# Optimization experiments

Measured on AMD Instinct MI355X. Metric: run time of the kernel, lower is better.

Reference implementation:

```python
import jax, jax.numpy as jnp
import numpy as np

D_MODEL = 1024
NUM_HEADS = 16
HEAD_DIM = D_MODEL // NUM_HEADS
B, S = 2, 2048


def setup_inputs() -> dict:
    key = jax.random.key(0)
    ks = jax.random.split(key, 16)
    sd = 1.0 / np.sqrt(D_MODEL)
    def lin(k):
        kw, kb = jax.random.split(k)
        W = jax.random.uniform(kw, (D_MODEL, D_MODEL), jnp.float32, -sd, sd)
        b = jax.random.uniform(kb, (D_MODEL,), jnp.float32, -sd, sd)
        return W, b
    Wq, bq = lin(ks[0]); Wk, bk = lin(ks[1]); Wv, bv = lin(ks[2]); Wo, bo = lin(ks[3])
    return {
        'q': jax.random.normal(ks[4], (B, S, D_MODEL), jnp.float32),
        'k': jax.random.normal(ks[5], (B, S, D_MODEL), jnp.float32),
        'v': jax.random.normal(ks[6], (B, S, D_MODEL), jnp.float32),
        'phase': jax.random.normal(ks[7], (B,), jnp.float32),
        'Wq': Wq, 'bq': bq, 'Wk': Wk, 'bk': bk, 'Wv': Wv, 'bv': bv, 'Wo': Wo, 'bo': bo,
        'phase_coupling': jnp.zeros((1, NUM_HEADS, 1, 1), jnp.float32),
        'attention_scale': jnp.ones((1,), jnp.float32),
        'stability_factor': jnp.ones((1,), jnp.float32),
    }


def reference(q, k, v, phase, Wq, bq, Wk, bk, Wv, bv, Wo, bo,
              phase_coupling, attention_scale, stability_factor):
    batch, seq, _ = q.shape
    scale = HEAD_DIM ** -0.5

    def split_heads(x):  # [B,S,D] -> [B,H,S,hd]
        return x.reshape(batch, -1, NUM_HEADS, HEAD_DIM).transpose(0, 2, 1, 3)

    qh = split_heads(q @ Wq.T + bq)
    kh = split_heads(k @ Wk.T + bk)
    vh = split_heads(v @ Wv.T + bv)

    scores = jnp.einsum('bhqd,bhkd->bhqk', qh, kh) * (scale * attention_scale)
    # phase modulation: phase [B] -> [B,1,1,1]; scores *= 1 + coupling*sin(phase)
    phase_factor = jnp.sin(phase)[:, None, None, None]
    scores = scores * (1.0 + phase_coupling * phase_factor)

    attn_weights = jax.nn.softmax(scores, axis=-1)  # dropout is identity in eval
    out = jnp.einsum('bhqk,bhkd->bhqd', attn_weights, vh)
    out = out.transpose(0, 2, 1, 3).reshape(batch, seq, D_MODEL)
    out = (out @ Wo.T + bo) * stability_factor
    return out, attn_weights
```

## Files before the change

kernel.cpp:

```cpp
#include <hip/hip_runtime.h>
#include <hip/hip_bf16.h>
#include <cstdint>
#include <cstddef>
#include <cmath>

#define NH 16
#define HD 64
#define SS 2048
#define DM 1024
#define MTOT 4096

typedef __attribute__((ext_vector_type(8))) short short8;
typedef __attribute__((ext_vector_type(4))) float float4v;
typedef __attribute__((ext_vector_type(4))) int int4v;
typedef __attribute__((ext_vector_type(4))) unsigned short ushort4v;

__device__ __forceinline__ unsigned short f2bf(float f){
  unsigned int u = __builtin_bit_cast(unsigned int, f);
  u += 0x7FFFu + ((u >> 16) & 1u);
  return (unsigned short)(u >> 16);
}

__device__ __forceinline__ void gload16(const void* g, void* l){
  __builtin_amdgcn_global_load_lds((const __attribute__((address_space(1))) void*)g,
                                   (__attribute__((address_space(3))) void*)l, 16, 0, 0);
}

__global__ __launch_bounds__(256) void cvt3_kernel(
    const float* __restrict__ s0, const float* __restrict__ s1, const float* __restrict__ s2,
    unsigned short* __restrict__ d0, unsigned short* __restrict__ d1, unsigned short* __restrict__ d2,
    int n){
  const int z = blockIdx.z;
  const float* src = z==0 ? s0 : (z==1 ? s1 : s2);
  unsigned short* dst = z==0 ? d0 : (z==1 ? d1 : d2);
  for (int i = (blockIdx.x*blockDim.x + threadIdx.x)*4; i < n; i += gridDim.x*blockDim.x*4){
    float4v v = *reinterpret_cast<const float4v*>(src + i);
    ushort4v o;
    o.x = f2bf(v.x); o.y = f2bf(v.y); o.z = f2bf(v.z); o.w = f2bf(v.w);
    *reinterpret_cast<ushort4v*>(dst + i) = o;
  }
}

__global__ __launch_bounds__(256) void cvt4_kernel(
    const float* __restrict__ s0, const float* __restrict__ s1,
    const float* __restrict__ s2, const float* __restrict__ s3,
    unsigned short* __restrict__ d0, unsigned short* __restrict__ d1,
    unsigned short* __restrict__ d2, unsigned short* __restrict__ d3,
    int n){
  const int z = blockIdx.z;
  const float* src = z==0 ? s0 : (z==1 ? s1 : (z==2 ? s2 : s3));
  unsigned short* dst = z==0 ? d0 : (z==1 ? d1 : (z==2 ? d2 : d3));
  for (int i = (blockIdx.x*blockDim.x + threadIdx.x)*4; i < n; i += gridDim.x*blockDim.x*4){
    float4v v = *reinterpret_cast<const float4v*>(src + i);
    ushort4v o;
    o.x = f2bf(v.x); o.y = f2bf(v.y); o.z = f2bf(v.z); o.w = f2bf(v.w);
    *reinterpret_cast<ushort4v*>(dst + i) = o;
  }
}

__global__ __launch_bounds__(256) void gemm_proj(
    const unsigned short* __restrict__ X0, const unsigned short* __restrict__ X1, const unsigned short* __restrict__ X2,
    const unsigned short* __restrict__ W0, const unsigned short* __restrict__ W1, const unsigned short* __restrict__ W2,
    const float* __restrict__ b0, const float* __restrict__ b1, const float* __restrict__ b2,
    unsigned short* __restrict__ O0, unsigned short* __restrict__ O1, unsigned short* __restrict__ O2){
  __shared__ unsigned short Alds[128*32];
  __shared__ unsigned short Blds[128*32];
  const int z = blockIdx.z;
  const unsigned short* A  = z==0 ? X0 : (z==1 ? X1 : X2);
  const unsigned short* Bw = z==0 ? W0 : (z==1 ? W1 : W2);
  const float* bias        = z==0 ? b0 : (z==1 ? b1 : b2);
  unsigned short* outp     = z==0 ? O0 : (z==1 ? O1 : O2);
  const bool vmode = (z == 2);
  const int K = DM;
  const int t = threadIdx.x;
  const int l = t & 63;
  const int w = t >> 6;
  const int m0 = blockIdx.y * 128, n0 = blockIdx.x * 128;
  const int wm = (w & 1)*64, wn = (w >> 1)*64;
  const int srow = t >> 2;
  const int scol = (t & 3)*8;
  const int lr = l & 15, lg = l >> 4;
  float4v acc[4][4] = {};
  for (int k0 = 0; k0 < K; k0 += 32){
    __syncthreads();
    gload16(A  + (size_t)(m0 + srow     )*K + k0 + scol, Alds + t*8);
    gload16(A  + (size_t)(m0 + srow + 64)*K + k0 + scol, Alds + 2048 + t*8);
    gload16(Bw + (size_t)(n0 + srow     )*K + k0 + scol, Blds + t*8);
    gload16(Bw + (size_t)(n0 + srow + 64)*K + k0 + scol, Blds + 2048 + t*8);
    asm volatile("s_waitcnt vmcnt(0)" ::: "memory");
    __syncthreads();
    short8 afrag[4], bfrag[4];
    #pragma unroll
    for (int mb = 0; mb < 4; ++mb)
      afrag[mb] = *reinterpret_cast<const short8*>(Alds + (wm + mb*16 + lr)*32 + lg*8);
    #pragma unroll
    for (int nb = 0; nb < 4; ++nb)
      bfrag[nb] = *reinterpret_cast<const short8*>(Blds + (wn + nb*16 + lr)*32 + lg*8);
    #pragma unroll
    for (int mb = 0; mb < 4; ++mb)
      #pragma unroll
      for (int nb = 0; nb < 4; ++nb)
        acc[mb][nb] = __builtin_amdgcn_mfma_f32_16x16x32_bf16(afrag[mb], bfrag[nb], acc[mb][nb], 0, 0, 0);
  }
  #pragma unroll
  for (int mb = 0; mb < 4; ++mb){
    #pragma unroll
    for (int nb = 0; nb < 4; ++nb){
      const int gn = n0 + wn + nb*16 + lr;
      const float biasv = bias[gn];
      #pragma unroll
      for (int r = 0; r < 4; ++r){
        const int gm = m0 + wm + mb*16 + lg*4 + r;
        float v = acc[mb][nb][r] + biasv;
        const int b_ = gm >> 11, s_ = gm & 2047, h_ = gn >> 6, d_ = gn & 63;
        if (!vmode)
          outp[((size_t)(b_*NH + h_)*SS + s_)*HD + d_] = f2bf(v);
        else
          outp[((size_t)(b_*NH + h_)*HD + d_)*SS + s_] = f2bf(v);
      }
    }
  }
}

__global__ __launch_bounds__(256) void gemm_out(const unsigned short* __restrict__ A,
                                                const unsigned short* __restrict__ Bw,
                                                const float* __restrict__ bias,
                                                float* __restrict__ outp,
                                                const float* __restrict__ oscale_p){
  __shared__ unsigned short Alds[128*32];
  __shared__ unsigned short Blds[128*32];
  const int K = DM, N = DM;
  const int t = threadIdx.x;
  const int l = t & 63;
  const int w = t >> 6;
  const int m0 = blockIdx.y * 128, n0 = blockIdx.x * 128;
  const int wm = (w & 1)*64, wn = (w >> 1)*64;
  const int srow = t >> 2;
  const int scol = (t & 3)*8;
  const int lr = l & 15, lg = l >> 4;
  float4v acc[4][4] = {};
  for (int k0 = 0; k0 < K; k0 += 32){
    __syncthreads();
    gload16(A  + (size_t)(m0 + srow     )*K + k0 + scol, Alds + t*8);
    gload16(A  + (size_t)(m0 + srow + 64)*K + k0 + scol, Alds + 2048 + t*8);
    gload16(Bw + (size_t)(n0 + srow     )*K + k0 + scol, Blds + t*8);
    gload16(Bw + (size_t)(n0 + srow + 64)*K + k0 + scol, Blds + 2048 + t*8);
    asm volatile("s_waitcnt vmcnt(0)" ::: "memory");
    __syncthreads();
    short8 afrag[4], bfrag[4];
    #pragma unroll
    for (int mb = 0; mb < 4; ++mb)
      afrag[mb] = *reinterpret_cast<const short8*>(Alds + (wm + mb*16 + lr)*32 + lg*8);
    #pragma unroll
    for (int nb = 0; nb < 4; ++nb)
      bfrag[nb] = *reinterpret_cast<const short8*>(Blds + (wn + nb*16 + lr)*32 + lg*8);
    #pragma unroll
    for (int mb = 0; mb < 4; ++mb)
      #pragma unroll
      for (int nb = 0; nb < 4; ++nb)
        acc[mb][nb] = __builtin_amdgcn_mfma_f32_16x16x32_bf16(afrag[mb], bfrag[nb], acc[mb][nb], 0, 0, 0);
  }
  const float osc = oscale_p[0];
  #pragma unroll
  for (int mb = 0; mb < 4; ++mb){
    #pragma unroll
    for (int nb = 0; nb < 4; ++nb){
      const int gn = n0 + wn + nb*16 + lr;
      const float biasv = bias[gn];
      #pragma unroll
      for (int r = 0; r < 4; ++r){
        const int gm = m0 + wm + mb*16 + lg*4 + r;
        outp[(size_t)gm*N + gn] = (acc[mb][nb][r] + biasv) * osc;
      }
    }
  }
}

__global__ __launch_bounds__(256, 4) void attn_kernel(
    const unsigned short* __restrict__ Qh,
    const unsigned short* __restrict__ Kh,
    const unsigned short* __restrict__ Vt,
    unsigned short* __restrict__ AO,
    float* __restrict__ attnW,
    const float* __restrict__ phase,
    const float* __restrict__ pc,
    const float* __restrict__ ascale)
{
  __shared__ float mred[4][32], lred[4][32];
  __shared__ __attribute__((aligned(16))) float ored[4][32*32];

  const int t = threadIdx.x;
  const int w = t >> 6, l = t & 63;
  const int lr = l & 15, lg = l >> 4;
  const int bh = blockIdx.x, qt = blockIdx.y;
  const int b = bh >> 4, h = bh & 15;
  const int q0 = qt*32;
  const float scale_eff = 0.125f * ascale[0] * (1.0f + pc[h] * sinf(phase[b]));

  const unsigned short* qbase = Qh + ((size_t)bh*SS + q0 + lr)*HD + lg*8;
  short8 aq[2][2];
  aq[0][0] = *reinterpret_cast<const short8*>(qbase);
  aq[0][1] = *reinterpret_cast<const short8*>(qbase + 32);
  aq[1][0] = *reinterpret_cast<const short8*>(qbase + 16*HD);
  aq[1][1] = *reinterpret_cast<const short8*>(qbase + 16*HD + 32);

  const int tbase = w * 512;
  const unsigned short* kbase = Kh + ((size_t)bh*SS + tbase + lr)*HD + lg*8;

  float m[2] = {-1e30f, -1e30f}, lsum[2] = {0.f, 0.f};
  #pragma unroll 2
  for (int tb = 0; tb < 32; ++tb){
    const unsigned short* kp = kbase + (size_t)tb*16*HD;
    short8 bk0 = *reinterpret_cast<const short8*>(kp);
    short8 bk1 = *reinterpret_cast<const short8*>(kp + 32);
    #pragma unroll
    for (int qs = 0; qs < 2; ++qs){
      float4v pacc = {};
      pacc = __builtin_amdgcn_mfma_f32_16x16x32_bf16(bk0, aq[qs][0], pacc, 0, 0, 0);
      pacc = __builtin_amdgcn_mfma_f32_16x16x32_bf16(bk1, aq[qs][1], pacc, 0, 0, 0);
      const float s0 = pacc[0]*scale_eff, s1 = pacc[1]*scale_eff;
      const float s2 = pacc[2]*scale_eff, s3 = pacc[3]*scale_eff;
      const float smax = fmaxf(fmaxf(s0, s1), fmaxf(s2, s3));
      const float nm = fmaxf(m[qs], smax);
      lsum[qs] = lsum[qs]*__expf(m[qs] - nm)
               + __expf(s0 - nm) + __expf(s1 - nm) + __expf(s2 - nm) + __expf(s3 - nm);
      m[qs] = nm;
    }
  }
  #pragma unroll
  for (int mask = 16; mask < 64; mask <<= 1){
    #pragma unroll
    for (int qs = 0; qs < 2; ++qs){
      float om = __shfl_xor(m[qs], mask, 64);
      float ol = __shfl_xor(lsum[qs], mask, 64);
      float nm = fmaxf(m[qs], om);
      lsum[qs] = lsum[qs]*__expf(m[qs] - nm) + ol*__expf(om - nm);
      m[qs] = nm;
    }
  }
  if (l < 16){
    mred[w][lr] = m[0];      lred[w][lr] = lsum[0];
    mred[w][16+lr] = m[1];   lred[w][16+lr] = lsum[1];
  }
  __syncthreads();
  float rm[2], rrl[2];
  #pragma unroll
  for (int qs = 0; qs < 2; ++qs){
    const int row = qs*16 + lr;
    float fm = mred[0][row], fl = lred[0][row];
    #pragma unroll
    for (int ww = 1; ww < 4; ++ww){
      float om = mred[ww][row], ol = lred[ww][row];
      float nm = fmaxf(fm, om);
      fl = fl*__expf(fm - nm) + ol*__expf(om - nm);
      fm = nm;
    }
    rm[qs] = fm; rrl[qs] = 1.0f/fl;
  }

  float4v oacc[2][4] = {};
  float* gwq0 = attnW + ((size_t)bh*SS + q0 + lr)*SS + tbase;
  float* gwq1 = gwq0 + (size_t)16*SS;
  const unsigned short* vbase = Vt + ((size_t)bh*HD + lr)*SS + tbase + lg*8;
  const int idxA = (((lg & 1)*2)*16 + lr)*4;
  const int idxB = idxA + 64;
  const bool hi = (lg >= 2);

  for (int tp = 0; tp < 16; ++tp){
    const int tloc = tp*32;
    const unsigned short* kpA = kbase + (size_t)tloc*HD;
    short8 k0A = *reinterpret_cast<const short8*>(kpA);
    short8 k1A = *reinterpret_cast<const short8*>(kpA + 32);
    short8 k0B = *reinterpret_cast<const short8*>(kpA + 16*HD);
    short8 k1B = *reinterpret_cast<const short8*>(kpA + 16*HD + 32);
    short8 bv[4];
    #pragma unroll
    for (int dt = 0; dt < 4; ++dt)
      bv[dt] = *reinterpret_cast<const short8*>(vbase + (size_t)(dt*16)*SS + tloc);

    #pragma unroll
    for (int qs = 0; qs < 2; ++qs){
      float4v pA = {};
      pA = __builtin_amdgcn_mfma_f32_16x16x32_bf16(k0A, aq[qs][0], pA, 0, 0, 0);
      pA = __builtin_amdgcn_mfma_f32_16x16x32_bf16(k1A, aq[qs][1], pA, 0, 0, 0);
      float4v pB = {};
      pB = __builtin_amdgcn_mfma_f32_16x16x32_bf16(k0B, aq[qs][0], pB, 0, 0, 0);
      pB = __builtin_amdgcn_mfma_f32_16x16x32_bf16(k1B, aq[qs][1], pB, 0, 0, 0);
      float4v eA, eB;
      eA.x = __expf(pA[0]*scale_eff - rm[qs])*rrl[qs];
      eA.y = __expf(pA[1]*scale_eff - rm[qs])*rrl[qs];
      eA.z = __expf(pA[2]*scale_eff - rm[qs])*rrl[qs];
      eA.w = __expf(pA[3]*scale_eff - rm[qs])*rrl[qs];
      eB.x = __expf(pB[0]*scale_eff - rm[qs])*rrl[qs];
      eB.y = __expf(pB[1]*scale_eff - rm[qs])*rrl[qs];
      eB.z = __expf(pB[2]*scale_eff - rm[qs])*rrl[qs];
      eB.w = __expf(pB[3]*scale_eff - rm[qs])*rrl[qs];
      const int w0A = ((int)f2bf(eA.y) << 16) | (int)f2bf(eA.x);
      const int w1A = ((int)f2bf(eA.w) << 16) | (int)f2bf(eA.z);
      const int w0B = ((int)f2bf(eB.y) << 16) | (int)f2bf(eB.x);
      const int w1B = ((int)f2bf(eB.w) << 16) | (int)f2bf(eB.z);

      const int a0 = __builtin_amdgcn_ds_bpermute(idxA, w0A);
      const int b0 = __builtin_amdgcn_ds_bpermute(idxA, w0B);
      const int a1 = __builtin_amdgcn_ds_bpermute(idxA, w1A);
      const int b1 = __builtin_amdgcn_ds_bpermute(idxA, w1B);
      const int a2 = __builtin_amdgcn_ds_bpermute(idxB, w0A);
      const int b2 = __builtin_amdgcn_ds_bpermute(idxB, w0B);
      const int a3 = __builtin_amdgcn_ds_bpermute(idxB, w1A);
      const int b3 = __builtin_amdgcn_ds_bpermute(idxB, w1B);
      int4v words;
      words.x = hi ? b0 : a0;
      words.y = hi ? b1 : a1;
      words.z = hi ? b2 : a2;
      words.w = hi ? b3 : a3;
      const short8 pa = __builtin_bit_cast(short8, words);

      #pragma unroll
      for (int dt = 0; dt < 4; ++dt)
        oacc[qs][dt] = __builtin_amdgcn_mfma_f32_16x16x32_bf16(pa, bv[dt], oacc[qs][dt], 0, 0, 0);

      float* gw = qs ? gwq1 : gwq0;
      *reinterpret_cast<float4v*>(gw + tloc + lg*4) = eA;
      *reinterpret_cast<float4v*>(gw + tloc + 16 + lg*4) = eB;
    }
  }

  #pragma unroll
  for (int c = 0; c < 2; ++c){
    if (c) __syncthreads();
    #pragma unroll
    for (int qs = 0; qs < 2; ++qs)
      #pragma unroll
      for (int dl = 0; dl < 2; ++dl)
        #pragma unroll
        for (int r = 0; r < 4; ++r)
          ored[w][(qs*16 + lg*4 + r)*32 + dl*16 + lr] = oacc[qs][c*2 + dl][r];
    __syncthreads();
    const int row = t >> 3, c4 = (t & 7);
    const float4v* o0 = reinterpret_cast<const float4v*>(&ored[0][0]);
    const int fi = row*8 + c4;
    float4v s = o0[fi];
    s += o0[fi + 256];
    s += o0[fi + 512];
    s += o0[fi + 768];
    ushort4v o4;
    o4.x = f2bf(s.x); o4.y = f2bf(s.y); o4.z = f2bf(s.z); o4.w = f2bf(s.w);
    *reinterpret_cast<ushort4v*>(AO + ((size_t)b*SS + q0 + row)*DM + h*HD + c*32 + c4*4) = o4;
  }
}

extern "C" void kernel_launch(void* const* d_in, const int* in_sizes, int n_in,
                              void* d_out, int out_size, void* d_ws, size_t ws_size,
                              hipStream_t stream){
  const float* q      = (const float*)d_in[0];
  const float* k      = (const float*)d_in[1];
  const float* v      = (const float*)d_in[2];
  const float* phase  = (const float*)d_in[3];
  const float* Wq     = (const float*)d_in[4];
  const float* bq     = (const float*)d_in[5];
  const float* Wk     = (const float*)d_in[6];
  const float* bk     = (const float*)d_in[7];
  const float* Wv     = (const float*)d_in[8];
  const float* bv     = (const float*)d_in[9];
  const float* Wo     = (const float*)d_in[10];
  const float* bo     = (const float*)d_in[11];
  const float* pc     = (const float*)d_in[12];
  const float* ascale = (const float*)d_in[13];
  const float* stab   = (const float*)d_in[14];

  unsigned short* Xq  = (unsigned short*)d_ws;
  unsigned short* Xk  = Xq  + 4194304;
  unsigned short* Xv  = Xk  + 4194304;
  unsigned short* Wqb = Xv  + 4194304;
  unsigned short* Wkb = Wqb + 1048576;
  unsigned short* Wvb = Wkb + 1048576;
  unsigned short* Wob = Wvb + 1048576;
  unsigned short* Qh  = Wob + 1048576;
  unsigned short* Kh  = Qh  + 4194304;
  unsigned short* Vt  = Kh  + 4194304;
  unsigned short* AO  = Vt  + 4194304;

  float* out0  = (float*)d_out;
  float* attnW = out0 + (size_t)MTOT*DM;

  cvt3_kernel<<<dim3(512,1,3), 256, 0, stream>>>(q, k, v, Xq, Xk, Xv, MTOT*DM);
  cvt4_kernel<<<dim3(128,1,4), 256, 0, stream>>>(Wq, Wk, Wv, Wo, Wqb, Wkb, Wvb, Wob, DM*DM);

  gemm_proj<<<dim3(DM/128, MTOT/128, 3), 256, 0, stream>>>(
      Xq, Xk, Xv, Wqb, Wkb, Wvb, bq, bk, bv, Qh, Kh, Vt);

  attn_kernel<<<dim3(32, SS/32, 1), 256, 0, stream>>>(Qh, Kh, Vt, AO, attnW,
                                                      phase, pc, ascale);

  gemm_out<<<dim3(DM/128, MTOT/128, 1), 256, 0, stream>>>(AO, Wob, bo, out0, stab);
}
```

Measured before the change: 315.6 us.

## Coalesce attention-weight stores via shuffles and feed PV MFMA directly

Attention-weight writes are reorganised with cross-lane shuffles so that each group of 8 lanes writes one full 128-byte row segment, and they use nontemporal stores, to cut scattered write traffic on the large attnW output. When the 16x16x16 bf16 MFMA builtin is available, P is fed straight from registers to the PV MFMA, which removes the ds_bpermute repacking at the cost of twice as many MFMAs and narrower V loads. The occupancy hint in launch bounds is raised from 4 to 6, which may force register spills. The added shuffles cost extra cross-lane work per tile.

```diff
diff --git a/kernel.cpp b/kernel.cpp
--- a/kernel.cpp
+++ b/kernel.cpp
@@ -11,9 +11,19 @@
 #define MTOT 4096
 
 typedef __attribute__((ext_vector_type(8))) short short8;
+typedef __attribute__((ext_vector_type(4))) short short4v;
 typedef __attribute__((ext_vector_type(4))) float float4v;
 typedef __attribute__((ext_vector_type(4))) int int4v;
 typedef __attribute__((ext_vector_type(4))) unsigned short ushort4v;
+
+#if defined(__has_builtin)
+# if __has_builtin(__builtin_amdgcn_mfma_f32_16x16x16bf16_1k)
+#  define PV_DIRECT 1
+# endif
+#endif
+#ifndef PV_DIRECT
+# define PV_DIRECT 0
+#endif
 
 __device__ __forceinline__ unsigned short f2bf(float f){
   unsigned int u = __builtin_bit_cast(unsigned int, f);
@@ -176,7 +186,7 @@
   }
 }
 
-__global__ __launch_bounds__(256, 4) void attn_kernel(
+__global__ __launch_bounds__(256, 6) void attn_kernel(
     const unsigned short* __restrict__ Qh,
     const unsigned short* __restrict__ Kh,
     const unsigned short* __restrict__ Vt,
@@ -259,12 +269,19 @@
   }
 
   float4v oacc[2][4] = {};
-  float* gwq0 = attnW + ((size_t)bh*SS + q0 + lr)*SS + tbase;
-  float* gwq1 = gwq0 + (size_t)16*SS;
-  const unsigned short* vbase = Vt + ((size_t)bh*HD + lr)*SS + tbase + lg*8;
+  float* gws0 = attnW + ((size_t)bh*SS + q0)*SS + tbase;
+  float* gws1 = gws0 + (size_t)16*SS;
+  const int row0 = l >> 3;
+  const int cgs  = l & 7;
+  const int src_base = ((cgs & 3) << 4) + row0;
+#if PV_DIRECT
+  const unsigned short* vbase4 = Vt + ((size_t)bh*HD + lr)*SS + tbase + lg*4;
+#else
+  const unsigned short* vbase8 = Vt + ((size_t)bh*HD + lr)*SS + tbase + lg*8;
   const int idxA = (((lg & 1)*2)*16 + lr)*4;
   const int idxB = idxA + 64;
   const bool hi = (lg >= 2);
+#endif
 
   for (int tp = 0; tp < 16; ++tp){
     const int tloc = tp*32;
@@ -273,10 +290,12 @@
     short8 k1A = *reinterpret_cast<const short8*>(kpA + 32);
     short8 k0B = *reinterpret_cast<const short8*>(kpA + 16*HD);
     short8 k1B = *reinterpret_cast<const short8*>(kpA + 16*HD + 32);
+#if !PV_DIRECT
     short8 bv[4];
     #pragma unroll
     for (int dt = 0; dt < 4; ++dt)
-      bv[dt] = *reinterpret_cast<const short8*>(vbase + (size_t)(dt*16)*SS + tloc);
+      bv[dt] = *reinterpret_cast<const short8*>(vbase8 + (size_t)(dt*16)*SS + tloc);
+#endif
 
     #pragma unroll
     for (int qs = 0; qs < 2; ++qs){
@@ -295,11 +314,25 @@
       eB.y = __expf(pB[1]*scale_eff - rm[qs])*rrl[qs];
       eB.z = __expf(pB[2]*scale_eff - rm[qs])*rrl[qs];
       eB.w = __expf(pB[3]*scale_eff - rm[qs])*rrl[qs];
+
+#if PV_DIRECT
+      short4v paA, paB;
+      paA[0]=(short)f2bf(eA.x); paA[1]=(short)f2bf(eA.y);
+      paA[2]=(short)f2bf(eA.z); paA[3]=(short)f2bf(eA.w);
+      paB[0]=(short)f2bf(eB.x); paB[1]=(short)f2bf(eB.y);
+      paB[2]=(short)f2bf(eB.z); paB[3]=(short)f2bf(eB.w);
+      #pragma unroll
+      for (int dt = 0; dt < 4; ++dt){
+        const short4v vfA = *reinterpret_cast<const short4v*>(vbase4 + (size_t)(dt*16)*SS + tloc);
+        const short4v vfB = *reinterpret_cast<const short4v*>(vbase4 + (size_t)(dt*16)*SS + tloc + 16);
+        oacc[qs][dt] = __builtin_amdgcn_mfma_f32_16x16x16bf16_1k(paA, vfA, oacc[qs][dt], 0, 0, 0);
+        oacc[qs][dt] = __builtin_amdgcn_mfma_f32_16x16x16bf16_1k(paB, vfB, oacc[qs][dt], 0, 0, 0);
+      }
+#else
       const int w0A = ((int)f2bf(eA.y) << 16) | (int)f2bf(eA.x);
       const int w1A = ((int)f2bf(eA.w) << 16) | (int)f2bf(eA.z);
       const int w0B = ((int)f2bf(eB.y) << 16) | (int)f2bf(eB.x);
       const int w1B = ((int)f2bf(eB.w) << 16) | (int)f2bf(eB.z);
-
       const int a0 = __builtin_amdgcn_ds_bpermute(idxA, w0A);
       const int b0 = __builtin_amdgcn_ds_bpermute(idxA, w0B);
       const int a1 = __builtin_amdgcn_ds_bpermute(idxA, w1A);
@@ -314,14 +347,29 @@
       words.z = hi ? b2 : a2;
       words.w = hi ? b3 : a3;
       const short8 pa = __builtin_bit_cast(short8, words);
-
       #pragma unroll
       for (int dt = 0; dt < 4; ++dt)
         oacc[qs][dt] = __builtin_amdgcn_mfma_f32_16x16x32_bf16(pa, bv[dt], oacc[qs][dt], 0, 0, 0);
-
-      float* gw = qs ? gwq1 : gwq0;
-      *reinterpret_cast<float4v*>(gw + tloc + lg*4) = eA;
-      *reinterpret_cast<float4v*>(gw + tloc + 16 + lg*4) = eB;
+#endif
+
+      float* gws = qs ? gws1 : gws0;
+      #pragma unroll
+      for (int rep = 0; rep < 2; ++rep){
+        const int src = src_base + rep*8;
+        float4v st;
+        {
+          const float fa0 = __shfl(eA.x, src, 64), fb0 = __shfl(eB.x, src, 64);
+          const float fa1 = __shfl(eA.y, src, 64), fb1 = __shfl(eB.y, src, 64);
+          const float fa2 = __shfl(eA.z, src, 64), fb2 = __shfl(eB.z, src, 64);
+          const float fa3 = __shfl(eA.w, src, 64), fb3 = __shfl(eB.w, src, 64);
+          st.x = (cgs < 4) ? fa0 : fb0;
+          st.y = (cgs < 4) ? fa1 : fb1;
+          st.z = (cgs < 4) ? fa2 : fb2;
+          st.w = (cgs < 4) ? fa3 : fb3;
+        }
+        __builtin_nontemporal_store(st,
+          reinterpret_cast<float4v*>(gws + (size_t)(row0 + rep*8)*SS + tloc + cgs*4));
+      }
     }
   }
 
```

After: 563.1 us. +78.4%, slower.
